# Kernel optimization log

Hardware: AMD Instinct MI355X
Metric: run time of the kernel (lower is better)

## Reference

```python
import jax, jax.numpy as jnp
import numpy as np

N_WG = 512      # waveguides n
N_COL = 512     # mesh columns
M = N_WG // 2   # node slots per column (odd columns have one masked dummy)
N_NODE = N_COL * M
B = 8192        # batch of input fields
PI4 = np.pi / 4


def build_mesh_indices():
    """Rectangular (Clements-style) mesh: per-column (top, bottom, mask) arrays."""
    top = np.zeros((N_COL, M), np.int32)
    bottom = np.zeros((N_COL, M), np.int32)
    mask = np.zeros((N_COL, M), np.int32)
    for c in range(N_COL):
        if c % 2 == 0:
            t = np.arange(0, N_WG, 2, dtype=np.int32)
            top[c], bottom[c], mask[c] = t, t + 1, 1
        else:
            t = np.arange(1, N_WG - 1, 2, dtype=np.int32)
            k = len(t)
            top[c, :k], bottom[c, :k], mask[c, :k] = t, t + 1, 1
            # masked dummy slot uses otherwise-unused rows 0 and N_WG-1
            top[c, k:], bottom[c, k:] = 0, N_WG - 1
    return jnp.asarray(top), jnp.asarray(bottom), jnp.asarray(mask)


def setup_inputs() -> dict:
    key = jax.random.key(0)
    ks = jax.random.split(key, 6)
    top, bottom, mask = build_mesh_indices()
    return {
        "x": jax.random.normal(ks[0], (N_WG, B), dtype=jnp.float32),
        "thetas": 2 * np.pi * jax.random.uniform(ks[1], (N_NODE,), dtype=jnp.float32),
        "phis": 2 * np.pi * jax.random.uniform(ks[2], (N_NODE,), dtype=jnp.float32),
        "gammas": 2 * np.pi * jax.random.uniform(ks[3], (N_WG,), dtype=jnp.float32),
        "bs_errors": 0.01 * jax.random.normal(ks[4], (N_NODE, 2), dtype=jnp.float32),
        "loss_errors": -0.1 * jax.random.uniform(ks[5], (N_NODE, 2), dtype=jnp.float32),
        "top": top, "bottom": bottom, "mask": mask,
    }


def _dc_terms(bs_errors, loss_errors, side):
    """_parallel_dc: per-node directional-coupler 2x2 elements [N,4] complex."""
    ins = jnp.exp(jnp.log(10.0) * loss_errors[:, side] / 20.0)
    e = bs_errors[:, side]
    s, c = jnp.sin(PI4 + e), jnp.cos(PI4 + e)
    t11 = (ins * s).astype(jnp.complex64)
    t12 = ins * (1j * c)
    t21 = (1j * c).astype(jnp.complex64)
    t22 = s.astype(jnp.complex64)
    return jnp.stack([t11, t12, t21, t22], axis=-1)


def _transform(v, T, t, b, m):
    """_parallel_transform: masked 2x2 gather-multiply-scatter. T: [M,4] complex."""
    vt, vb = v[t], v[b]
    one_m = 1.0 - m
    s11 = (T[:, 0] * m + one_m)[:, None]
    s12 = (T[:, 1] * m)[:, None]
    s21 = (T[:, 2] * m)[:, None]
    s22 = (T[:, 3] * m + one_m)[:, None]
    return v.at[t].set(s11 * vt + s21 * vb).at[b].set(s12 * vt + s22 * vb)


def reference(x, thetas, phis, gammas, bs_errors, loss_errors, top, bottom, mask):
    # input gamma phase screen, then propagate through all mesh columns
    v = x.astype(jnp.complex64) * jnp.exp(1j * gammas)[:, None]          # [n, B]
    left = _dc_terms(bs_errors, loss_errors, 0).reshape(N_COL, M, 4)
    right = _dc_terms(bs_errors, loss_errors, 1).reshape(N_COL, M, 4)
    th = thetas.reshape(N_COL, M)
    ph = phis.reshape(N_COL, M)
    mf = mask.astype(jnp.float32)

    def column(v, xs):
        t, b, m, thc, phc, L, R = xs
        # PhaseStyle.TOP, forward: phi -> left DC -> theta -> right DC
        v = v.at[t].multiply(jnp.exp(1j * phc * m)[:, None])
        v = _transform(v, L, t, b, m)
        v = v.at[t].multiply(jnp.exp(1j * thc * m)[:, None])
        v = _transform(v, R, t, b, m)
        return v, None

    v, _ = jax.lax.scan(column, v, (top, bottom, mf, th, ph, left, right))
    return jnp.stack([v.real, v.imag])  # [2, n, B]
```

## Files before the change

### kernel.cpp

```cpp
#include <hip/hip_runtime.h>
#include <math.h>

#define BATCH 8192
#define NROW 512
#define NCOL 512
#define MNODE 256

typedef __attribute__((ext_vector_type(8))) short bf16x8;
typedef __attribute__((ext_vector_type(4))) float f32x4;

__device__ __forceinline__ short2 split1(float x) {
  unsigned u = __float_as_uint(x);
  short h = (short)(u >> 16);
  float r = x - __uint_as_float(u & 0xffff0000u);
  short l = (short)(__float_as_uint(r) >> 16);
  return make_short2(h, l);
}

__global__ __launch_bounds__(256) void precomp_kernel(
    const float* __restrict__ thetas, const float* __restrict__ phis,
    const float* __restrict__ bse, const float* __restrict__ lse,
    float4* __restrict__ pp) {
  int n = blockIdx.x * 256 + threadIdx.x;
  float th = thetas[n], ph = phis[n];
  float e0 = bse[2 * n + 0], e1 = bse[2 * n + 1];
  float l0 = lse[2 * n + 0], l1 = lse[2 * n + 1];
  const float K = 0.16609640474436813f;
  float ins0 = exp2f(l0 * K), ins1 = exp2f(l1 * K);
  const float PI4 = 0.7853981633974483f;
  float s0, c0, s1, c1, sp, cp, st, ct;
  sincosf(PI4 + e0, &s0, &c0);
  sincosf(PI4 + e1, &s1, &c1);
  sincosf(ph, &sp, &cp);
  sincosf(th, &st, &ct);
  float AL = ins0 * s0, C1L = c0, C2L = ins0 * c0, SL = s0;
  float AR = ins1 * s1, C1R = c1, C2R = ins1 * c1, SR = s1;
  float a11r = AL * cp,   a11i = AL * sp;
  float a12r = 0.f,       a12i = C1L;
  float a21r = -C2L * sp, a21i = C2L * cp;
  float a22r = SL,        a22i = 0.f;
  float b11r = a11r * ct - a11i * st, b11i = a11r * st + a11i * ct;
  float b12r = a12r * ct - a12i * st, b12i = a12r * st + a12i * ct;
  float n11r = AR * b11r - C1R * a21i;
  float n11i = AR * b11i + C1R * a21r;
  float n12r = AR * b12r - C1R * a22i;
  float n12i = AR * b12i + C1R * a22r;
  float n21r = -C2R * b11i + SR * a21r;
  float n21i =  C2R * b11r + SR * a21i;
  float n22r = -C2R * b12i + SR * a22r;
  float n22i =  C2R * b12r + SR * a22i;
  pp[2 * n + 0] = make_float4(n11r, n11i, n12r, n12i);
  pp[2 * n + 1] = make_float4(n21r, n21i, n22r, n22i);
}

__device__ __forceinline__ void proc_pair(float& vtr, float& vti, float& vbr, float& vbi,
                                          const float4 q0, const float4 q1) {
  float tr = q0.x * vtr - q0.y * vti + q0.z * vbr - q0.w * vbi;
  float ti = q0.x * vti + q0.y * vtr + q0.z * vbi + q0.w * vbr;
  float br = q1.x * vtr - q1.y * vti + q1.z * vbr - q1.w * vbi;
  float bi = q1.x * vti + q1.y * vtr + q1.z * vbi + q1.w * vbr;
  vtr = tr; vti = ti; vbr = br; vbi = bi;
}

__device__ __forceinline__ int swz(int b) { return b ^ ((b >> 3) & 7); }

__global__ __launch_bounds__(256) void compose_kernel(
    const float* __restrict__ gammas, const float4* __restrict__ pp,
    float* __restrict__ Tsegs, int pairs_per_seg) {
  __shared__ float4 buf[2][1024];
  __shared__ float ep[1024][5];

  const int tid  = threadIdx.x;
  const int lane = tid & 63;
  const int w    = tid >> 6;
  const int seg  = blockIdx.x >> 7;
  const int g    = blockIdx.x & 127;
  const int col  = g * 4 + w;

  const float4* ps = pp + (size_t)seg * pairs_per_seg * 1024;
  float* T = Tsegs + (size_t)seg * (1024 * NROW);

  float vr[8], vi[8];
#pragma unroll
  for (int r = 0; r < 8; ++r) {
    const int row = lane * 8 + r;
    vr[r] = 0.f; vi[r] = 0.f;
    if (row == col) {
      if (seg == 0) {
        float sg, cg;
        sincosf(gammas[row], &sg, &cg);
        vr[r] = cg; vi[r] = sg;
      } else {
        vr[r] = 1.f;
      }
    }
  }

  {
    const int sw = swz(tid);
#pragma unroll
    for (int k = 0; k < 4; ++k)
      buf[0][256 * k + sw] = ps[256 * k + tid];
  }
  __syncthreads();

#pragma unroll 1
  for (int p = 0; p < pairs_per_seg; ++p) {
    const int b = p & 1;

    float4 f0, f1, f2, f3;
    if (p < pairs_per_seg - 1) {
      const float4* src = ps + (size_t)(p + 1) * 1024;
      f0 = src[tid]; f1 = src[256 + tid]; f2 = src[512 + tid]; f3 = src[768 + tid];
    }

    float4 pe[8], po[8], pu1;
    {
      const int base = 8 * lane;
      const int l7 = lane & 7;
#pragma unroll
      for (int j = 0; j < 8; ++j) pe[j] = buf[b][base + (j ^ l7)];
#pragma unroll
      for (int j = 0; j < 8; ++j) po[j] = buf[b][512 + base + (j ^ l7)];
      const int lm = (lane == 0) ? 0 : lane - 1;
      pu1 = buf[b][512 + 8 * lm + (7 ^ (lm & 7))];
    }

#pragma unroll
    for (int k = 0; k < 4; ++k)
      proc_pair(vr[2 * k], vi[2 * k], vr[2 * k + 1], vi[2 * k + 1],
                pe[2 * k], pe[2 * k + 1]);

#pragma unroll
    for (int k = 0; k < 3; ++k)
      proc_pair(vr[2 * k + 1], vi[2 * k + 1], vr[2 * k + 2], vi[2 * k + 2],
                po[2 * k], po[2 * k + 1]);

    {
      float br = __shfl_down(vr[0], 1, 64);
      float bi = __shfl_down(vi[0], 1, 64);
      float tu = __shfl_up(vr[7], 1, 64);
      float tv = __shfl_up(vi[7], 1, 64);
      float nAr = po[6].x * vr[7] - po[6].y * vi[7] + po[6].z * br - po[6].w * bi;
      float nAi = po[6].x * vi[7] + po[6].y * vr[7] + po[6].z * bi + po[6].w * br;
      float nBr = pu1.x * tu - pu1.y * tv + pu1.z * vr[0] - pu1.w * vi[0];
      float nBi = pu1.x * tv + pu1.y * tu + pu1.z * vi[0] + pu1.w * vr[0];
      if (lane < 63) { vr[7] = nAr; vi[7] = nAi; }
      if (lane > 0)  { vr[0] = nBr; vi[0] = nBi; }
    }

    if (p < pairs_per_seg - 1) {
      const int sw = swz(tid);
      buf[1 - b][sw] = f0;
      buf[1 - b][256 + sw] = f1;
      buf[1 - b][512 + sw] = f2;
      buf[1 - b][768 + sw] = f3;
    }
    __syncthreads();
  }

#pragma unroll
  for (int r = 0; r < 8; ++r) {
    ep[lane * 8 + r][w] = vr[r];
    ep[512 + lane * 8 + r][w] = vi[r];
  }
  __syncthreads();
#pragma unroll
  for (int k = 0; k < 4; ++k) {
    const int i = k * 256 + tid;
    *(float4*)(T + (size_t)i * NROW + g * 4) =
        make_float4(ep[i][0], ep[i][1], ep[i][2], ep[i][3]);
  }
}

__global__ __launch_bounds__(256) void merge_mfma(
    const float* __restrict__ A0, const float* __restrict__ B0, float* __restrict__ C0,
    const float* __restrict__ A1, const float* __restrict__ B1, float* __restrict__ C1) {
  const float* A = blockIdx.z ? A1 : A0;
  const float* B = blockIdx.z ? B1 : B0;
  float*       C = blockIdx.z ? C1 : C0;

  __shared__ short sAh[64 * 40], sAl[64 * 40];

  const int tid = threadIdx.x;
  const int lane = tid & 63;
  const int w = tid >> 6;
  const int bm = blockIdx.y * 64;
  const int bn = blockIdx.x * 64;
  const int wm = (w & 1) * 32;
  const int wn = (w >> 1) * 32;
  const int q = lane >> 4;
  const int l15 = lane & 15;

  const int sm = tid >> 2;
  const int sk = (tid & 3) * 8;

  f32x4 acc[2][2];
#pragma unroll
  for (int i = 0; i < 2; ++i)
#pragma unroll
    for (int j = 0; j < 2; ++j) acc[i][j] = (f32x4){0.f, 0.f, 0.f, 0.f};

#pragma unroll 1
  for (int k0 = 0; k0 < 1024; k0 += 32) {
    {
      const int gm = bm + sm;
      const int gk = k0 + sk;
      const int r = gm & 511;
      const bool top = gm < 512;
      const bool left = gk < 512;
      const int col = gk & 511;
      const float* src = (top == left) ? (A + (size_t)r * 512)
                                       : (A + (size_t)(512 + r) * 512);
      const float sgn = (top && !left) ? -1.f : 1.f;
      float4 v0 = *(const float4*)(src + col);
      float4 v1 = *(const float4*)(src + col + 4);
      float vv[8] = {v0.x, v0.y, v0.z, v0.w, v1.x, v1.y, v1.z, v1.w};
      short h[8], l[8];
#pragma unroll
      for (int i = 0; i < 8; ++i) {
        short2 s = split1(sgn * vv[i]);
        h[i] = s.x; l[i] = s.y;
      }
      __syncthreads();
      *(bf16x8*)&sAh[sm * 40 + sk] = *(bf16x8*)h;
      *(bf16x8*)&sAl[sm * 40 + sk] = *(bf16x8*)l;
      __syncthreads();
    }

    bf16x8 bh[2], bl[2];
#pragma unroll
    for (int nt = 0; nt < 2; ++nt) {
      const float* bp = B + (size_t)(k0 + q * 8) * 512 + bn + wn + nt * 16 + l15;
      short hh[8], ll[8];
#pragma unroll
      for (int j = 0; j < 8; ++j) {
        short2 s = split1(bp[(size_t)j * 512]);
        hh[j] = s.x; ll[j] = s.y;
      }
      bh[nt] = *(bf16x8*)hh;
      bl[nt] = *(bf16x8*)ll;
    }

    bf16x8 ah[2], al[2];
#pragma unroll
    for (int mt = 0; mt < 2; ++mt) {
      const int m = wm + mt * 16 + l15;
      ah[mt] = *(const bf16x8*)&sAh[m * 40 + q * 8];
      al[mt] = *(const bf16x8*)&sAl[m * 40 + q * 8];
    }

#pragma unroll
    for (int mt = 0; mt < 2; ++mt)
#pragma unroll
      for (int nt = 0; nt < 2; ++nt) {
        acc[mt][nt] = __builtin_amdgcn_mfma_f32_16x16x32_bf16(ah[mt], bh[nt], acc[mt][nt], 0, 0, 0);
        acc[mt][nt] = __builtin_amdgcn_mfma_f32_16x16x32_bf16(ah[mt], bl[nt], acc[mt][nt], 0, 0, 0);
        acc[mt][nt] = __builtin_amdgcn_mfma_f32_16x16x32_bf16(al[mt], bh[nt], acc[mt][nt], 0, 0, 0);
      }
  }

#pragma unroll
  for (int mt = 0; mt < 2; ++mt)
#pragma unroll
    for (int nt = 0; nt < 2; ++nt)
#pragma unroll
      for (int r = 0; r < 4; ++r) {
        const int gm = bm + wm + mt * 16 + q * 4 + r;
        const int gn = bn + wn + nt * 16 + l15;
        C[(size_t)gm * 512 + gn] = acc[mt][nt][r];
      }
}

__global__ __launch_bounds__(256) void gemm_mfma(
    const float* __restrict__ A, const float* __restrict__ B,
    float* __restrict__ C) {
  __shared__ short sAh[128 * 40], sAl[128 * 40];

  const int tid = threadIdx.x;
  const int lane = tid & 63;
  const int w = tid >> 6;
  const int bm = blockIdx.y * 128;
  const int bn = blockIdx.x * 128;
  const int wm = (w & 1) * 64;
  const int wn = (w >> 1) * 64;
  const int q = lane >> 4;
  const int l15 = lane & 15;

  const int sm = tid >> 1;
  const int sk = (tid & 1) * 16;
  const float* Ap = A + (size_t)(bm + sm) * 512 + sk;

  f32x4 acc[4][4];
#pragma unroll
  for (int i = 0; i < 4; ++i)
#pragma unroll
    for (int j = 0; j < 4; ++j) acc[i][j] = (f32x4){0.f, 0.f, 0.f, 0.f};

  float4 pa[4];
#pragma unroll
  for (int i = 0; i < 4; ++i) pa[i] = *(const float4*)(Ap + i * 4);

#pragma unroll 1
  for (int k0 = 0; k0 < 512; k0 += 32) {
    {
      short h[16], l[16];
#pragma unroll
      for (int i = 0; i < 16; ++i) {
        short2 s = split1(((const float*)pa)[i]);
        h[i] = s.x; l[i] = s.y;
      }
      __syncthreads();
      *(bf16x8*)&sAh[sm * 40 + sk]     = *(bf16x8*)&h[0];
      *(bf16x8*)&sAh[sm * 40 + sk + 8] = *(bf16x8*)&h[8];
      *(bf16x8*)&sAl[sm * 40 + sk]     = *(bf16x8*)&l[0];
      *(bf16x8*)&sAl[sm * 40 + sk + 8] = *(bf16x8*)&l[8];
      __syncthreads();
    }

    if (k0 + 32 < 512) {
#pragma unroll
      for (int i = 0; i < 4; ++i) pa[i] = *(const float4*)(Ap + k0 + 32 + i * 4);
    }

    bf16x8 bh[4], bl[4];
#pragma unroll
    for (int nt = 0; nt < 4; ++nt) {
      const float* bp = B + (size_t)(k0 + q * 8) * BATCH + bn + wn + nt * 16 + l15;
      short hh[8], ll[8];
#pragma unroll
      for (int j = 0; j < 8; ++j) {
        short2 s = split1(bp[(size_t)j * BATCH]);
        hh[j] = s.x; ll[j] = s.y;
      }
      bh[nt] = *(bf16x8*)hh;
      bl[nt] = *(bf16x8*)ll;
    }

    bf16x8 ah[4], al[4];
#pragma unroll
    for (int mt = 0; mt < 4; ++mt) {
      const int m = wm + mt * 16 + l15;
      ah[mt] = *(const bf16x8*)&sAh[m * 40 + q * 8];
      al[mt] = *(const bf16x8*)&sAl[m * 40 + q * 8];
    }

#pragma unroll
    for (int mt = 0; mt < 4; ++mt)
#pragma unroll
      for (int nt = 0; nt < 4; ++nt) {
        acc[mt][nt] = __builtin_amdgcn_mfma_f32_16x16x32_bf16(ah[mt], bh[nt], acc[mt][nt], 0, 0, 0);
        acc[mt][nt] = __builtin_amdgcn_mfma_f32_16x16x32_bf16(ah[mt], bl[nt], acc[mt][nt], 0, 0, 0);
        acc[mt][nt] = __builtin_amdgcn_mfma_f32_16x16x32_bf16(al[mt], bh[nt], acc[mt][nt], 0, 0, 0);
      }
  }

#pragma unroll
  for (int mt = 0; mt < 4; ++mt)
#pragma unroll
    for (int nt = 0; nt < 4; ++nt)
#pragma unroll
      for (int r = 0; r < 4; ++r) {
        const int gm = bm + wm + mt * 16 + q * 4 + r;
        const int gn = bn + wn + nt * 16 + l15;
        C[(size_t)gm * BATCH + gn] = acc[mt][nt][r];
      }
}

extern "C" void kernel_launch(void* const* d_in, const int* in_sizes, int n_in,
                              void* d_out, int out_size, void* d_ws, size_t ws_size,
                              hipStream_t stream) {
  const float* x      = (const float*)d_in[0];
  const float* thetas = (const float*)d_in[1];
  const float* phis   = (const float*)d_in[2];
  const float* gammas = (const float*)d_in[3];
  const float* bse    = (const float*)d_in[4];
  const float* lse    = (const float*)d_in[5];

  float* base = (float*)d_ws;
  float4* pp  = (float4*)d_ws;
  const size_t PPF   = 1048576;
  const size_t SEGSZ = 524288;

  int nseg;
  if (ws_size >= (size_t)14 * 1024 * 1024)      nseg = 4;
  else if (ws_size >= (size_t)8 * 1024 * 1024)  nseg = 2;
  else                                          nseg = 1;

  float* segs = base + PPF;
  float* Tf;

  precomp_kernel<<<512, 256, 0, stream>>>(thetas, phis, bse, lse, pp);
  compose_kernel<<<nseg * 128, 256, 0, stream>>>(gammas, pp, segs, 256 / nseg);

  if (nseg == 4) {
    float* T0  = segs + 0 * SEGSZ;
    float* T1  = segs + 1 * SEGSZ;
    float* T2  = segs + 2 * SEGSZ;
    float* T3  = segs + 3 * SEGSZ;
    float* T10 = base;
    float* T32 = base + SEGSZ;
    Tf = segs + 4 * SEGSZ;
    merge_mfma<<<dim3(8, 16, 2), 256, 0, stream>>>(T1, T0, T10, T3, T2, T32);
    merge_mfma<<<dim3(8, 16, 1), 256, 0, stream>>>(T32, T10, Tf, T32, T10, Tf);
  } else if (nseg == 2) {
    float* T0 = segs + 0 * SEGSZ;
    float* T1 = segs + 1 * SEGSZ;
    Tf = base;
    merge_mfma<<<dim3(8, 16, 1), 256, 0, stream>>>(T1, T0, Tf, T1, T0, Tf);
  } else {
    Tf = segs;
  }

  gemm_mfma<<<dim3(BATCH / 128, 8), 256, 0, stream>>>(Tf, x, (float*)d_out);
}
```

Measured before the change: 257.7 us.

## Restrict compose work to light-cone of nonzero matrix entries per column

The compose kernel builds each column of the segment transfer matrix starting from a unit vector, so only rows within a growing light-cone around the starting row can be nonzero after p column pairs. Lanes outside that cone now skip their LDS parameter reads and complex 2x2 updates. Global prefetches and LDS stores are also limited to the parameter range the workgroup can need. This saves memory traffic and ALU work in early iterations, but it depends on the cone bounds being exact, and divergence within a wave may limit how much is actually saved.

```diff
diff --git a/kernel.cpp b/kernel.cpp
--- a/kernel.cpp
+++ b/kernel.cpp
@@ -76,6 +76,7 @@
   const int seg  = blockIdx.x >> 7;
   const int g    = blockIdx.x & 127;
   const int col  = g * 4 + w;
+  const int colmin = g * 4;
 
   const float4* ps = pp + (size_t)seg * pairs_per_seg * 1024;
   float* T = Tsegs + (size_t)seg * (1024 * NROW);
@@ -104,43 +105,58 @@
   }
   __syncthreads();
 
+  const int Lc = col >> 3;
+
 #pragma unroll 1
   for (int p = 0; p < pairs_per_seg; ++p) {
     const int b = p & 1;
 
+    const int HA = (p >> 2) + 3;
+    const bool act  = (lane >= Lc - HA)     && (lane <= Lc + HA);
+    const bool wide = (lane >= Lc - HA - 1) && (lane <= Lc + HA + 1);
+
     float4 f0, f1, f2, f3;
+    bool st0 = false, st1 = false;
     if (p < pairs_per_seg - 1) {
+      const int slo = colmin - 2 * p - 50;
+      const int shi = colmin + 2 * p + 53;
+      st0 = (tid + 1 >= slo) && (tid <= shi);
+      st1 = (tid + 257 >= slo) && (tid + 256 <= shi);
       const float4* src = ps + (size_t)(p + 1) * 1024;
-      f0 = src[tid]; f1 = src[256 + tid]; f2 = src[512 + tid]; f3 = src[768 + tid];
-    }
-
-    float4 pe[8], po[8], pu1;
-    {
+      if (st0) { f0 = src[tid];       f2 = src[512 + tid]; }
+      if (st1) { f1 = src[256 + tid]; f3 = src[768 + tid]; }
+    }
+
+    float4 pe[8], po[7], pu1;
+    if (act) {
       const int base = 8 * lane;
       const int l7 = lane & 7;
 #pragma unroll
       for (int j = 0; j < 8; ++j) pe[j] = buf[b][base + (j ^ l7)];
 #pragma unroll
-      for (int j = 0; j < 8; ++j) po[j] = buf[b][512 + base + (j ^ l7)];
+      for (int j = 0; j < 7; ++j) po[j] = buf[b][512 + base + (j ^ l7)];
       const int lm = (lane == 0) ? 0 : lane - 1;
       pu1 = buf[b][512 + 8 * lm + (7 ^ (lm & 7))];
-    }
-
-#pragma unroll
-    for (int k = 0; k < 4; ++k)
-      proc_pair(vr[2 * k], vi[2 * k], vr[2 * k + 1], vi[2 * k + 1],
-                pe[2 * k], pe[2 * k + 1]);
-
-#pragma unroll
-    for (int k = 0; k < 3; ++k)
-      proc_pair(vr[2 * k + 1], vi[2 * k + 1], vr[2 * k + 2], vi[2 * k + 2],
-                po[2 * k], po[2 * k + 1]);
-
-    {
-      float br = __shfl_down(vr[0], 1, 64);
-      float bi = __shfl_down(vi[0], 1, 64);
-      float tu = __shfl_up(vr[7], 1, 64);
-      float tv = __shfl_up(vi[7], 1, 64);
+
+#pragma unroll
+      for (int k = 0; k < 4; ++k)
+        proc_pair(vr[2 * k], vi[2 * k], vr[2 * k + 1], vi[2 * k + 1],
+                  pe[2 * k], pe[2 * k + 1]);
+
+#pragma unroll
+      for (int k = 0; k < 3; ++k)
+        proc_pair(vr[2 * k + 1], vi[2 * k + 1], vr[2 * k + 2], vi[2 * k + 2],
+                  po[2 * k], po[2 * k + 1]);
+    }
+
+    float br = 0.f, bi = 0.f, tu = 0.f, tv = 0.f;
+    if (wide) {
+      br = __shfl_down(vr[0], 1, 64);
+      bi = __shfl_down(vi[0], 1, 64);
+      tu = __shfl_up(vr[7], 1, 64);
+      tv = __shfl_up(vi[7], 1, 64);
+    }
+    if (act) {
       float nAr = po[6].x * vr[7] - po[6].y * vi[7] + po[6].z * br - po[6].w * bi;
       float nAi = po[6].x * vi[7] + po[6].y * vr[7] + po[6].z * bi + po[6].w * br;
       float nBr = pu1.x * tu - pu1.y * tv + pu1.z * vr[0] - pu1.w * vi[0];
@@ -151,10 +167,8 @@
 
     if (p < pairs_per_seg - 1) {
       const int sw = swz(tid);
-      buf[1 - b][sw] = f0;
-      buf[1 - b][256 + sw] = f1;
-      buf[1 - b][512 + sw] = f2;
-      buf[1 - b][768 + sw] = f3;
+      if (st0) { buf[1 - b][sw] = f0;       buf[1 - b][512 + sw] = f2; }
+      if (st1) { buf[1 - b][256 + sw] = f1; buf[1 - b][768 + sw] = f3; }
     }
     __syncthreads();
   }
```

Result: no change. 260.1 us (+1.0%).
